# Performance work log

Measured on AMD Instinct MI355X. Metric: run time of the kernel, lower is better.

## Reference

```python
import jax, jax.numpy as jnp
import numpy as np

D = 1024; H = 16; DH = 64; L = 4; N0 = 512; N1 = 512; NF = 16; B = 4; FF = 2730
FUSION = -1; GLOBAL = -2

# static token-type masks (zorro=True path)
_tt = np.concatenate([np.zeros(N0, np.int64), np.ones(N1, np.int64), np.full(NF, FUSION, np.int64)])
_allowed = (_tt[:, None] == _tt[None, :]) | (_tt[:, None] == FUSION)
ATTN_MASK = jnp.asarray(~_allowed)  # True = masked, shape [N, N]
_rt = np.array([0, 1, FUSION, GLOBAL], np.int64)
_pool_allowed = (_rt[:, None] == _tt[None, :]) | (_rt[:, None] == GLOBAL)
POOL_MASK = jnp.asarray(~_pool_allowed)  # [4, N]


def setup_inputs() -> dict:
    key = jax.random.key(0)
    ks = jax.random.split(key, 14)
    s = 0.02
    return {
        'm0': jax.random.normal(ks[0], (B, N0, D), jnp.float32),
        'm1': jax.random.normal(ks[1], (B, N1, D), jnp.float32),
        'fusion_tokens': jax.random.normal(ks[2], (NF, D), jnp.float32),
        'return_tokens': jax.random.normal(ks[3], (4, D), jnp.float32),
        'ln_gamma': jnp.ones((L, D), jnp.float32),
        'wq': jax.random.normal(ks[4], (L, D, H * DH), jnp.float32) * s,
        'wkv': jax.random.normal(ks[5], (L, D, 2 * H * DH), jnp.float32) * s,
        'wo': jax.random.normal(ks[6], (L, H * DH, D), jnp.float32) * s,
        'ff_w1': jax.random.normal(ks[7], (L, D, 2 * FF), jnp.float32) * s,
        'ff_w2': jax.random.normal(ks[8], (L, FF, D), jnp.float32) * s,
        'pool_wq': jax.random.normal(ks[9], (D, H * DH), jnp.float32) * s,
        'pool_wkv': jax.random.normal(ks[10], (D, 2 * H * DH), jnp.float32) * s,
        'pool_wo': jax.random.normal(ks[11], (H * DH, D), jnp.float32) * s,
        'final_gamma': jnp.ones((D,), jnp.float32),
    }


def _ln(x, g):
    mu = jnp.mean(x, axis=-1, keepdims=True)
    var = jnp.mean(jnp.square(x - mu), axis=-1, keepdims=True)
    return (x - mu) * jax.lax.rsqrt(var + 1e-5) * g


def _heads(t):  # [b, n, h*d] -> [b, h, n, d]
    b, n, _ = t.shape
    return t.reshape(b, n, H, DH).transpose(0, 2, 1, 3)


def _attn(x, ctx, wq, wkv, wo, mask):
    q = _heads(x @ wq) * (DH ** -0.5)
    k, v = map(_heads, jnp.split(ctx @ wkv, 2, axis=-1))
    sim = jnp.einsum('bhid,bhjd->bhij', q, k)
    sim = jnp.where(mask, -jnp.finfo(sim.dtype).max, sim)
    attn = jax.nn.softmax(sim, axis=-1)
    out = jnp.einsum('bhij,bhjd->bhid', attn, v)
    b, h, n, d = out.shape
    return out.transpose(0, 2, 1, 3).reshape(b, n, h * d) @ wo


def _ff(x, w1, w2):
    val, gate = jnp.split(x @ w1, 2, axis=-1)
    return (jax.nn.gelu(gate, approximate=False) * val) @ w2


def reference(m0, m1, fusion_tokens, return_tokens, ln_gamma, wq, wkv, wo, ff_w1, ff_w2, pool_wq, pool_wkv, pool_wo, final_gamma):
    b = m0.shape[0]
    fus = jnp.broadcast_to(fusion_tokens[None], (b, NF, D))
    tokens = jnp.concatenate([m0, m1, fus], axis=1)  # [B, N, D]
    for l in range(L):
        h = _ln(tokens, ln_gamma[l])
        tokens = _attn(h, h, wq[l], wkv[l], wo[l], ATTN_MASK) + tokens
        h = _ln(tokens, ln_gamma[l])
        tokens = _ff(h, ff_w1[l], ff_w2[l]) + tokens
    tokens = _ln(tokens, final_gamma)
    q = jnp.broadcast_to(return_tokens[None], (b, 4, D))
    pooled = _attn(q, tokens, pool_wq, pool_wkv, pool_wo, POOL_MASK) + return_tokens[None]
    return pooled
```

## Files before the change

### kernel.cpp

```cpp
#include <hip/hip_runtime.h>
#include <stdint.h>


#define DEV __device__ __forceinline__

typedef unsigned short u16;
typedef __attribute__((ext_vector_type(8))) __bf16 bf16x8;
typedef __attribute__((ext_vector_type(4))) float floatx4;

DEV u16 f2bf(float f) {
  union { float f; unsigned u; } v; v.f = f;
  return (u16)((v.u + 0x7fffu + ((v.u >> 16) & 1u)) >> 16);
}
DEV float bf2f(u16 s) {
  union { unsigned u; float f; } v; v.u = ((unsigned)s) << 16;
  return v.f;
}

#define MFMA(a, b, c) __builtin_amdgcn_mfma_f32_16x16x32_bf16(a, b, c, 0, 0, 0)

DEV void gld16(const u16* g, u16* l) {
  __builtin_amdgcn_global_load_lds((__attribute__((address_space(1))) void*)g,
                                   (__attribute__((address_space(3))) void*)l,
                                   16, 0, 0);
}

DEV int vperm32(int j) {
  return (((j >> 2) & 3) << 3) | (j & 3) | (((j >> 4) & 1) << 2);
}

#define MREAL 4160
#define MPAD  4224
#define NPAD  1056
#define FFP   2816
#define FF2P  5632

__global__ __launch_bounds__(256) void transpose_cvt(
    const float* __restrict__ in, u16* __restrict__ out,
    int Kin, int N, int Kstride) {
  __shared__ float tile[32][33];
  const int k0 = blockIdx.x * 32, n0 = blockIdx.y * 32;
  const int tx = threadIdx.x, ty = threadIdx.y;
#pragma unroll
  for (int i = 0; i < 4; i++) {
    int k = k0 + ty + i * 8;
    tile[ty + i * 8][tx] = (k < Kin) ? in[(int64_t)k * N + n0 + tx] : 0.f;
  }
  __syncthreads();
#pragma unroll
  for (int i = 0; i < 4; i++) {
    int n = n0 + ty + i * 8;
    int k = k0 + tx;
    if (k < Kstride) out[(int64_t)n * Kstride + k] = f2bf(tile[tx][ty + i * 8]);
  }
}

__global__ __launch_bounds__(256) void transpose_w1(
    const float* __restrict__ in, u16* __restrict__ out) {
  __shared__ float tile[32][33];
  const int k0 = blockIdx.x * 32;
  const int r0 = blockIdx.y * 32;
  const int tx = threadIdx.x, ty = threadIdx.y;
  const int vb = (r0 >> 5) << 4;
  const int vi = vb + (tx & 15);
  const int c = (tx < 16) ? vi : 2730 + vi;
  const bool valid = vi < 2730;
#pragma unroll
  for (int i = 0; i < 4; i++) {
    int k = k0 + ty + i * 8;
    tile[ty + i * 8][tx] = valid ? in[(int64_t)k * 5460 + c] : 0.f;
  }
  __syncthreads();
#pragma unroll
  for (int i = 0; i < 4; i++) {
    int rl = ty + i * 8;
    out[(int64_t)(r0 + rl) * 1024 + k0 + tx] = f2bf(tile[tx][rl]);
  }
}

__global__ __launch_bounds__(256) void build_tokens_k(
    const float* __restrict__ m0p, const float* __restrict__ m1p,
    const float* __restrict__ fus, float* __restrict__ tokens) {
  const int n = blockIdx.x, b = blockIdx.y, t = threadIdx.x;
  const float* src = (n < 512) ? m0p + ((int64_t)b * 512 + n) * 1024
                   : (n < 1024) ? m1p + ((int64_t)b * 512 + (n - 512)) * 1024
                                : fus + (int64_t)(n - 1024) * 1024;
  float4 v = ((const float4*)src)[t];
  ((float4*)(tokens + ((int64_t)b * 1040 + n) * 1024))[t] = v;
}

__global__ __launch_bounds__(256) void ln_k(const float* __restrict__ x,
                                            const float* __restrict__ gamma,
                                            u16* __restrict__ out) {
  const int r = blockIdx.x, t = threadIdx.x;
  const float4 v = ((const float4*)(x + (int64_t)r * 1024))[t];
  float s = v.x + v.y + v.z + v.w;
  float q = v.x * v.x + v.y * v.y + v.z * v.z + v.w * v.w;
#pragma unroll
  for (int off = 32; off >= 1; off >>= 1) {
    s += __shfl_xor(s, off);
    q += __shfl_xor(q, off);
  }
  __shared__ float red[8];
  const int w = t >> 6, l = t & 63;
  if (l == 0) { red[w] = s; red[4 + w] = q; }
  __syncthreads();
  s = red[0] + red[1] + red[2] + red[3];
  q = red[4] + red[5] + red[6] + red[7];
  const float mu = s * (1.f / 1024.f);
  const float var = q * (1.f / 1024.f) - mu * mu;
  const float rs = rsqrtf(var + 1e-5f);
  const float4 g = ((const float4*)gamma)[t];
  u16* op = out + (int64_t)r * 1024 + t * 4;
  op[0] = f2bf((v.x - mu) * rs * g.x);
  op[1] = f2bf((v.y - mu) * rs * g.y);
  op[2] = f2bf((v.z - mu) * rs * g.z);
  op[3] = f2bf((v.w - mu) * rs * g.w);
}

enum { EPI_QKV = 0, EPI_KV = 1, EPI_TOKADD = 2, EPI_GG = 3 };

template <int EPI>
__global__ __launch_bounds__(256) void gemm_bt(
    const u16* __restrict__ A, const u16* __restrict__ Bt,
    int Kstr, int Mreal,
    float* __restrict__ tokens, u16* __restrict__ oq, u16* __restrict__ ok,
    u16* __restrict__ ovT, u16* __restrict__ oh2) {
  __shared__ __align__(16) u16 lA[2][128 * 64];
  __shared__ __align__(16) u16 lB[2][128 * 64];
  const int t = threadIdx.x;
  const int w = t >> 6, l = t & 63;
  const int lane16 = l & 15, quad = l >> 4;
  const int m0 = blockIdx.y * 128, n0 = blockIdx.x * 128;
  const int wm = (w >> 1) * 64, wn = (w & 1) * 64;

  const int Klen = Kstr / gridDim.z;
  const int koff = blockIdx.z * Klen;

  const floatx4 fz = {0.f, 0.f, 0.f, 0.f};
  floatx4 acc[4][4];
#pragma unroll
  for (int i = 0; i < 4; i++)
#pragma unroll
    for (int j = 0; j < 4; j++) acc[i][j] = fz;

  const int rowS = t >> 3;
  const int scol = (((t & 7) ^ (rowS & 7)) << 3);
  const u16* gAs = A + (int64_t)(m0 + rowS) * Kstr + koff + scol;
  const u16* gBs = Bt + (int64_t)(n0 + rowS) * Kstr + koff + scol;
  const int64_t csk = (int64_t)32 * Kstr;

  const int rsw = lane16 & 7;
  const int cp0 = ((quad ^ rsw) << 3);
  const int cp1 = (((quad + 4) ^ rsw) << 3);

  auto stage = [&](int buf, int kt) {
    const u16* ga = gAs + kt;
    const u16* gb = gBs + kt;
    u16* la = &lA[buf][0] + t * 8;
    u16* lb = &lB[buf][0] + t * 8;
#pragma unroll
    for (int c = 0; c < 4; c++) {
      gld16(ga + c * csk, la + c * 2048);
      gld16(gb + c * csk, lb + c * 2048);
    }
  };

  stage(0, 0);
  __syncthreads();
  int cur = 0;
  for (int kt = 0; kt < Klen; kt += 64) {
    if (kt + 64 < Klen) stage(cur ^ 1, kt + 64);
    const u16* la = &lA[cur][0] + (wm + lane16) * 64;
    const u16* lb = &lB[cur][0] + (wn + lane16) * 64;
    bf16x8 af[4], bf[4];
#pragma unroll
    for (int i = 0; i < 4; i++) af[i] = *(const bf16x8*)(la + i * 16 * 64 + cp0);
#pragma unroll
    for (int j = 0; j < 4; j++) bf[j] = *(const bf16x8*)(lb + j * 16 * 64 + cp0);
#pragma unroll
    for (int i = 0; i < 4; i++)
#pragma unroll
      for (int j = 0; j < 4; j++) acc[i][j] = MFMA(af[i], bf[j], acc[i][j]);
#pragma unroll
    for (int i = 0; i < 4; i++) af[i] = *(const bf16x8*)(la + i * 16 * 64 + cp1);
#pragma unroll
    for (int j = 0; j < 4; j++) bf[j] = *(const bf16x8*)(lb + j * 16 * 64 + cp1);
#pragma unroll
    for (int i = 0; i < 4; i++)
#pragma unroll
      for (int j = 0; j < 4; j++) acc[i][j] = MFMA(af[i], bf[j], acc[i][j]);
    __syncthreads();
    cur ^= 1;
  }

  if constexpr (EPI == EPI_TOKADD) {
    const bool atomic = gridDim.z > 1;
#pragma unroll
    for (int i = 0; i < 4; i++) {
      const int mb = m0 + wm + i * 16 + quad * 4;
#pragma unroll
      for (int reg = 0; reg < 4; reg++) {
        const int m = mb + reg;
        if (m < Mreal) {
          float* tp = tokens + (int64_t)m * 1024;
#pragma unroll
          for (int j = 0; j < 4; j++) {
            const int n = n0 + wn + j * 16 + lane16;
            if (atomic) atomicAdd(tp + n, acc[i][j][reg]);
            else tp[n] += acc[i][j][reg];
          }
        }
      }
    }
  } else if constexpr (EPI == EPI_QKV) {
#pragma unroll
    for (int i = 0; i < 4; i++) {
      const int mb = m0 + wm + i * 16 + quad * 4;
#pragma unroll
      for (int reg = 0; reg < 4; reg++) {
        const int m = mb + reg;
        if (m < Mreal) {
          const int b = m / 1040, rb = m % 1040;
          const int rbp = (rb & ~31) | vperm32(rb & 31);
#pragma unroll
          for (int j = 0; j < 4; j++) {
            const int n = n0 + wn + j * 16 + lane16;
            const float v = acc[i][j][reg];
            if (n < 1024) {
              const int hd = n >> 6, d = n & 63;
              oq[(((int64_t)b * 16 + hd) * NPAD + rb) * 64 + d] = f2bf(v * 0.125f);
            } else if (n < 2048) {
              const int n2 = n - 1024;
              const int hd = n2 >> 6, d = n2 & 63;
              ok[(((int64_t)b * 16 + hd) * NPAD + rb) * 64 + d] = f2bf(v);
            } else {
              const int n2 = n - 2048;
              const int hd = n2 >> 6, d = n2 & 63;
              ovT[(((int64_t)b * 16 + hd) * 64 + d) * NPAD + rbp] = f2bf(v);
            }
          }
        }
      }
    }
  } else if constexpr (EPI == EPI_KV) {
#pragma unroll
    for (int i = 0; i < 4; i++) {
      const int mb = m0 + wm + i * 16 + quad * 4;
#pragma unroll
      for (int reg = 0; reg < 4; reg++) {
        const int m = mb + reg;
        if (m < Mreal) {
          const int b = m / 1040, rb = m % 1040;
          const int rbp = (rb & ~31) | vperm32(rb & 31);
#pragma unroll
          for (int j = 0; j < 4; j++) {
            const int n = n0 + wn + j * 16 + lane16;
            const float v = acc[i][j][reg];
            if (n < 1024) {
              const int hd = n >> 6, d = n & 63;
              ok[(((int64_t)b * 16 + hd) * NPAD + rb) * 64 + d] = f2bf(v);
            } else {
              const int n2 = n - 1024;
              const int hd = n2 >> 6, d = n2 & 63;
              ovT[(((int64_t)b * 16 + hd) * 64 + d) * NPAD + rbp] = f2bf(v);
            }
          }
        }
      }
    }
  } else {
#pragma unroll
    for (int i = 0; i < 4; i++) {
      const int mb = m0 + wm + i * 16 + quad * 4;
#pragma unroll
      for (int reg = 0; reg < 4; reg++) {
        const int m = mb + reg;
        u16* hp = oh2 + (int64_t)m * FFP;
#pragma unroll
        for (int j = 0; j < 4; j += 2) {
          const float val = acc[i][j][reg];
          const float g = acc[i][j + 1][reg];
          const float ge = 0.5f * g * (1.f + erff(g * 0.70710678118654752f));
          const int vi = (((n0 + wn + j * 16) >> 5) << 4) + lane16;
          hp[vi] = f2bf(val * ge);
        }
      }
    }
  }
}

__global__ __launch_bounds__(256) void attn_k(const u16* __restrict__ qb,
                                              const u16* __restrict__ kb,
                                              const u16* __restrict__ vTb,
                                              u16* __restrict__ ao) {
  const int t = threadIdx.x, w = t >> 6, l = t & 63;
  const int lane16 = l & 15, quad = l >> 4;
  const int kvb = quad * 4;
  const int bh = blockIdx.y, b = bh >> 4, h = bh & 15;
  const int row0 = blockIdx.x * 64 + w * 16;
  if (row0 >= 1040) return;
  const int type = (row0 < 512) ? 0 : (row0 < 1024 ? 1 : 2);
  const int cbeg = (type == 1) ? 512 : 0;
  const int cend = (type == 0) ? 512 : (type == 1 ? 1024 : 1040);
  const int niter = (cend - cbeg + 31) >> 5;

  const u16* qp = qb + ((int64_t)bh * NPAD + row0 + lane16) * 64 + quad * 8;
  const bf16x8 a0 = *(const bf16x8*)qp;
  const bf16x8 a1 = *(const bf16x8*)(qp + 32);
  const u16* vbase = vTb + ((int64_t)bh * 64 + lane16) * NPAD + quad * 8;

  const floatx4 fz = {0.f, 0.f, 0.f, 0.f};
  floatx4 O[4] = {fz, fz, fz, fz};
  float mrow = -1e30f, lrow = 0.f;

  for (int it = 0; it < niter; ++it) {
    const int c0 = cbeg + it * 32;
    const u16* kp = kb + ((int64_t)bh * NPAD + c0 + lane16) * 64 + quad * 8;
    const bf16x8 b00 = *(const bf16x8*)kp;
    const bf16x8 b01 = *(const bf16x8*)(kp + 32);
    const bf16x8 b10 = *(const bf16x8*)(kp + 16 * 64);
    const bf16x8 b11 = *(const bf16x8*)(kp + 16 * 64 + 32);
    floatx4 s0 = MFMA(b00, a0, fz); s0 = MFMA(b01, a1, s0);
    floatx4 s1 = MFMA(b10, a0, fz); s1 = MFMA(b11, a1, s1);
    if (c0 + 32 > cend) {
#pragma unroll
      for (int r = 0; r < 4; r++) {
        if (c0 + kvb + r >= cend) s0[r] = -1e30f;
        if (c0 + 16 + kvb + r >= cend) s1[r] = -1e30f;
      }
    }
    float tm = fmaxf(fmaxf(fmaxf(s0[0], s0[1]), fmaxf(s0[2], s0[3])),
                     fmaxf(fmaxf(s1[0], s1[1]), fmaxf(s1[2], s1[3])));
    tm = fmaxf(tm, __shfl_xor(tm, 16));
    tm = fmaxf(tm, __shfl_xor(tm, 32));
    if (!__all(tm <= mrow)) {
      const float mn = fmaxf(mrow, tm);
      const float a_ = __expf(mrow - mn);
      mrow = mn;
      lrow *= a_;
      const float al0 = __shfl(a_, kvb + 0, 16);
      const float al1 = __shfl(a_, kvb + 1, 16);
      const float al2 = __shfl(a_, kvb + 2, 16);
      const float al3 = __shfl(a_, kvb + 3, 16);
#pragma unroll
      for (int dt = 0; dt < 4; dt++) {
        O[dt][0] *= al0; O[dt][1] *= al1; O[dt][2] *= al2; O[dt][3] *= al3;
      }
    }
    float p0[4], p1[4];
#pragma unroll
    for (int r = 0; r < 4; r++) {
      p0[r] = __expf(s0[r] - mrow);
      p1[r] = __expf(s1[r] - mrow);
    }
    float ps = ((p0[0] + p0[1]) + (p0[2] + p0[3])) +
               ((p1[0] + p1[1]) + (p1[2] + p1[3]));
    ps += __shfl_xor(ps, 16);
    ps += __shfl_xor(ps, 32);
    lrow += ps;
    union { bf16x8 v; u16 s[8]; } pf;
#pragma unroll
    for (int r = 0; r < 4; r++) {
      pf.s[r] = f2bf(p0[r]);
      pf.s[4 + r] = f2bf(p1[r]);
    }
#pragma unroll
    for (int dt = 0; dt < 4; dt++) {
      const bf16x8 bv = *(const bf16x8*)(vbase + (int64_t)dt * 16 * NPAD + c0);
      O[dt] = MFMA(pf.v, bv, O[dt]);
    }
  }
  float lr[4];
#pragma unroll
  for (int r = 0; r < 4; r++) lr[r] = __shfl(lrow, kvb + r, 16);
#pragma unroll
  for (int dt = 0; dt < 4; dt++)
#pragma unroll
    for (int r = 0; r < 4; r++) {
      const int row = row0 + kvb + r;
      ao[((int64_t)b * 1040 + row) * 1024 + h * 64 + dt * 16 + lane16] =
          f2bf(O[dt][r] / lr[r]);
    }
}

__global__ __launch_bounds__(256) void poolq_k(const float* __restrict__ rtk,
                                               const float* __restrict__ pwq,
                                               u16* __restrict__ qP) {
  const int r = blockIdx.y;
  const int n = blockIdx.x * 256 + threadIdx.x;
  if (r >= 4) { qP[(int64_t)r * 1024 + n] = 0; return; }
  const float* x = rtk + (int64_t)r * 1024;
  float acc = 0.f;
#pragma unroll 8
  for (int k = 0; k < 1024; k++) acc += x[k] * pwq[(int64_t)k * 1024 + n];
  qP[(int64_t)r * 1024 + n] = f2bf(acc * 0.125f);
}

DEV bool pvalid(int r, int c) {
  if (r == 0) return c < 512;
  if (r == 1) return (c >= 512) && (c < 1024);
  if (r == 2) return (c >= 1024) && (c < 1040);
  return c < 1040;
}

__global__ __launch_bounds__(64) void pool_attn_k(const u16* __restrict__ qP,
                                                  const u16* __restrict__ kb,
                                                  const u16* __restrict__ vTb,
                                                  u16* __restrict__ po) {
  const int l = threadIdx.x;
  const int lane16 = l & 15, quad = l >> 4;
  const int kvb = quad * 4;
  const int bh = blockIdx.x, b = bh >> 4, h = bh & 15;
  const u16* qp = qP + (int64_t)lane16 * 1024 + h * 64 + quad * 8;
  const bf16x8 a0 = *(const bf16x8*)qp;
  const bf16x8 a1 = *(const bf16x8*)(qp + 32);
  const u16* vbase = vTb + ((int64_t)bh * 64 + lane16) * NPAD + quad * 8;
  const floatx4 fz = {0.f, 0.f, 0.f, 0.f};
  floatx4 O[4] = {fz, fz, fz, fz};
  float mrow = -1e30f, lrow = 0.f;
  for (int it = 0; it < 33; ++it) {
    const int c0 = it * 32;
    const u16* kp = kb + ((int64_t)bh * NPAD + c0 + lane16) * 64 + quad * 8;
    const bf16x8 b00 = *(const bf16x8*)kp;
    const bf16x8 b01 = *(const bf16x8*)(kp + 32);
    const bf16x8 b10 = *(const bf16x8*)(kp + 16 * 64);
    const bf16x8 b11 = *(const bf16x8*)(kp + 16 * 64 + 32);
    floatx4 s0 = MFMA(b00, a0, fz); s0 = MFMA(b01, a1, s0);
    floatx4 s1 = MFMA(b10, a0, fz); s1 = MFMA(b11, a1, s1);
#pragma unroll
    for (int r = 0; r < 4; r++) {
      if (!pvalid(lane16, c0 + kvb + r)) s0[r] = -1e30f;
      if (!pvalid(lane16, c0 + 16 + kvb + r)) s1[r] = -1e30f;
    }
    float tm = fmaxf(fmaxf(fmaxf(s0[0], s0[1]), fmaxf(s0[2], s0[3])),
                     fmaxf(fmaxf(s1[0], s1[1]), fmaxf(s1[2], s1[3])));
    tm = fmaxf(tm, __shfl_xor(tm, 16));
    tm = fmaxf(tm, __shfl_xor(tm, 32));
    if (!__all(tm <= mrow)) {
      const float mn = fmaxf(mrow, tm);
      const float a_ = __expf(mrow - mn);
      mrow = mn;
      lrow *= a_;
      const float al0 = __shfl(a_, kvb + 0, 16);
      const float al1 = __shfl(a_, kvb + 1, 16);
      const float al2 = __shfl(a_, kvb + 2, 16);
      const float al3 = __shfl(a_, kvb + 3, 16);
#pragma unroll
      for (int dt = 0; dt < 4; dt++) {
        O[dt][0] *= al0; O[dt][1] *= al1; O[dt][2] *= al2; O[dt][3] *= al3;
      }
    }
    float p0[4], p1[4];
#pragma unroll
    for (int r = 0; r < 4; r++) {
      p0[r] = __expf(s0[r] - mrow);
      p1[r] = __expf(s1[r] - mrow);
    }
    float ps = ((p0[0] + p0[1]) + (p0[2] + p0[3])) +
               ((p1[0] + p1[1]) + (p1[2] + p1[3]));
    ps += __shfl_xor(ps, 16);
    ps += __shfl_xor(ps, 32);
    lrow += ps;
    union { bf16x8 v; u16 s[8]; } pf;
#pragma unroll
    for (int r = 0; r < 4; r++) {
      pf.s[r] = f2bf(p0[r]);
      pf.s[4 + r] = f2bf(p1[r]);
    }
#pragma unroll
    for (int dt = 0; dt < 4; dt++) {
      const bf16x8 bv = *(const bf16x8*)(vbase + (int64_t)dt * 16 * NPAD + c0);
      O[dt] = MFMA(pf.v, bv, O[dt]);
    }
  }
  float lr[4];
#pragma unroll
  for (int r = 0; r < 4; r++) lr[r] = __shfl(lrow, r, 16);
  if (quad == 0) {
#pragma unroll
    for (int dt = 0; dt < 4; dt++)
#pragma unroll
      for (int r = 0; r < 4; r++)
        po[((int64_t)b * 4 + r) * 1024 + h * 64 + dt * 16 + lane16] =
            f2bf(O[dt][r] / lr[r]);
  }
}

__global__ __launch_bounds__(256) void fout_k(const u16* __restrict__ po,
                                              const float* __restrict__ pwo,
                                              const float* __restrict__ rtk,
                                              float* __restrict__ out) {
  const int row = blockIdx.y;
  const int n = blockIdx.x * 256 + threadIdx.x;
  const u16* x = po + (int64_t)row * 1024;
  float acc = 0.f;
#pragma unroll 8
  for (int k = 0; k < 1024; k++) acc += bf2f(x[k]) * pwo[(int64_t)k * 1024 + n];
  out[(int64_t)row * 1024 + n] = acc + rtk[(int64_t)(row & 3) * 1024 + n];
}

extern "C" void kernel_launch(void* const* d_in, const int* in_sizes, int n_in,
                              void* d_out, int out_size, void* d_ws, size_t ws_size,
                              hipStream_t stream) {
  (void)in_sizes; (void)n_in; (void)out_size; (void)ws_size;
  const float* m0p  = (const float*)d_in[0];
  const float* m1p  = (const float*)d_in[1];
  const float* fus  = (const float*)d_in[2];
  const float* rtk  = (const float*)d_in[3];
  const float* lng  = (const float*)d_in[4];
  const float* wq   = (const float*)d_in[5];
  const float* wkv  = (const float*)d_in[6];
  const float* wo   = (const float*)d_in[7];
  const float* w1   = (const float*)d_in[8];
  const float* w2   = (const float*)d_in[9];
  const float* pwq  = (const float*)d_in[10];
  const float* pwkv = (const float*)d_in[11];
  const float* pwo  = (const float*)d_in[12];
  const float* fg   = (const float*)d_in[13];
  float* out = (float*)d_out;

  char* p = (char*)d_ws;
  auto alloc = [&](size_t bytes) -> char* {
    char* r = p;
    p += (bytes + 255) & ~(size_t)255;
    return r;
  };
  u16* warena = (u16*)alloc((size_t)FF2P * 1024 * 2);
  float* tokens = (float*)alloc((size_t)MREAL * 1024 * 4);
  u16* hbuf  = (u16*)alloc((size_t)MPAD * 1024 * 2);
  u16* qb    = (u16*)alloc((size_t)64 * NPAD * 64 * 2);
  u16* kbuf  = (u16*)alloc((size_t)64 * NPAD * 64 * 2);
  u16* vTbuf = (u16*)alloc((size_t)64 * NPAD * 64 * 2);
  u16* h2buf = qb;
  u16* qP    = (u16*)alloc((size_t)16 * 1024 * 2);
  u16* poolO = (u16*)alloc((size_t)16 * 1024 * 2);

  const dim3 tb(32, 8, 1);
  build_tokens_k<<<dim3(1040, 4), 256, 0, stream>>>(m0p, m1p, fus, tokens);

  for (int lyr = 0; lyr < 4; ++lyr) {
    ln_k<<<MREAL, 256, 0, stream>>>(tokens, lng + lyr * 1024, hbuf);
    transpose_cvt<<<dim3(32, 32), tb, 0, stream>>>(
        wq + (int64_t)lyr * 1024 * 1024, warena, 1024, 1024, 1024);
    transpose_cvt<<<dim3(32, 64), tb, 0, stream>>>(
        wkv + (int64_t)lyr * 1024 * 2048, warena + (size_t)1024 * 1024, 1024, 2048, 1024);
    gemm_bt<EPI_QKV><<<dim3(24, 33), 256, 0, stream>>>(
        hbuf, warena, 1024, MREAL, nullptr, qb, kbuf, vTbuf, nullptr);
    attn_k<<<dim3(17, 64), 256, 0, stream>>>(qb, kbuf, vTbuf, hbuf);
    transpose_cvt<<<dim3(32, 32), tb, 0, stream>>>(
        wo + (int64_t)lyr * 1024 * 1024, warena, 1024, 1024, 1024);
    gemm_bt<EPI_TOKADD><<<dim3(8, 33, 2), 256, 0, stream>>>(
        hbuf, warena, 1024, MREAL, tokens, nullptr, nullptr, nullptr, nullptr);
    ln_k<<<MREAL, 256, 0, stream>>>(tokens, lng + lyr * 1024, hbuf);
    transpose_w1<<<dim3(32, FF2P / 32), tb, 0, stream>>>(
        w1 + (int64_t)lyr * 1024 * 5460, warena);
    gemm_bt<EPI_GG><<<dim3(FF2P / 128, 33), 256, 0, stream>>>(
        hbuf, warena, 1024, MREAL, nullptr, nullptr, nullptr, nullptr, h2buf);
    transpose_cvt<<<dim3(FFP / 32, 32), tb, 0, stream>>>(
        w2 + (int64_t)lyr * 2730 * 1024, warena, 2730, 1024, FFP);
    gemm_bt<EPI_TOKADD><<<dim3(8, 33, 2), 256, 0, stream>>>(
        h2buf, warena, FFP, MREAL, tokens, nullptr, nullptr, nullptr, nullptr);
  }

  ln_k<<<MREAL, 256, 0, stream>>>(tokens, fg, hbuf);
  transpose_cvt<<<dim3(32, 64), tb, 0, stream>>>(pwkv, warena, 1024, 2048, 1024);
  gemm_bt<EPI_KV><<<dim3(16, 33), 256, 0, stream>>>(
      hbuf, warena, 1024, MREAL, nullptr, nullptr, kbuf, vTbuf, nullptr);
  poolq_k<<<dim3(4, 16), 256, 0, stream>>>(rtk, pwq, qP);
  pool_attn_k<<<64, 64, 0, stream>>>(qP, kbuf, vTbuf, poolO);
  fout_k<<<dim3(4, 16), 256, 0, stream>>>(poolO, pwo, rtk, out);
}
```

Baseline: 1.877 ms.

## Replace atomic split-K residual adds with delta buffers fused into LayerNorm

The split-K output and FF-down GEMMs now write plain partial results into separate delta buffers instead of atomically adding into the residual tokens. A new add_ln_k kernel sums the tokens with the deltas, writes the updated residual back, and applies the next LayerNorm in one pass. This is meant to remove atomic read-modify-write traffic and a separate residual read. In exchange it needs extra workspace and adds extra fp32 reads and writes, and it falls back to the old path when the workspace is too small.

Measured after the change: 1.802 ms. -4.0%, faster.

```diff
diff --git a/kernel.cpp b/kernel.cpp
--- a/kernel.cpp
+++ b/kernel.cpp
@@ -118,7 +118,47 @@
   op[3] = f2bf((v.w - mu) * rs * g.w);
 }
 
-enum { EPI_QKV = 0, EPI_KV = 1, EPI_TOKADD = 2, EPI_GG = 3 };
+__global__ __launch_bounds__(256) void add_ln_k(
+    float* __restrict__ x, const float* __restrict__ d0,
+    const float* __restrict__ d1, const float* __restrict__ gamma,
+    u16* __restrict__ out, int two, int writeback) {
+  const int r = blockIdx.x, t = threadIdx.x;
+  const int64_t off = (int64_t)r * 1024 + t * 4;
+  float4 v = *(const float4*)(x + off);
+  {
+    const float4 a = *(const float4*)(d0 + off);
+    v.x += a.x; v.y += a.y; v.z += a.z; v.w += a.w;
+  }
+  if (two) {
+    const float4 a = *(const float4*)(d1 + off);
+    v.x += a.x; v.y += a.y; v.z += a.z; v.w += a.w;
+  }
+  if (writeback) *(float4*)(x + off) = v;
+  float s = v.x + v.y + v.z + v.w;
+  float q = v.x * v.x + v.y * v.y + v.z * v.z + v.w * v.w;
+#pragma unroll
+  for (int off2 = 32; off2 >= 1; off2 >>= 1) {
+    s += __shfl_xor(s, off2);
+    q += __shfl_xor(q, off2);
+  }
+  __shared__ float red[8];
+  const int w = t >> 6, l = t & 63;
+  if (l == 0) { red[w] = s; red[4 + w] = q; }
+  __syncthreads();
+  s = red[0] + red[1] + red[2] + red[3];
+  q = red[4] + red[5] + red[6] + red[7];
+  const float mu = s * (1.f / 1024.f);
+  const float var = q * (1.f / 1024.f) - mu * mu;
+  const float rs = rsqrtf(var + 1e-5f);
+  const float4 g = ((const float4*)gamma)[t];
+  u16* op = out + (int64_t)r * 1024 + t * 4;
+  op[0] = f2bf((v.x - mu) * rs * g.x);
+  op[1] = f2bf((v.y - mu) * rs * g.y);
+  op[2] = f2bf((v.z - mu) * rs * g.z);
+  op[3] = f2bf((v.w - mu) * rs * g.w);
+}
+
+enum { EPI_QKV = 0, EPI_KV = 1, EPI_TOKADD = 2, EPI_GG = 3, EPI_DELTA = 4 };
 
 template <int EPI>
 __global__ __launch_bounds__(256) void gemm_bt(
@@ -209,6 +249,24 @@
             const int n = n0 + wn + j * 16 + lane16;
             if (atomic) atomicAdd(tp + n, acc[i][j][reg]);
             else tp[n] += acc[i][j][reg];
+          }
+        }
+      }
+    }
+  } else if constexpr (EPI == EPI_DELTA) {
+    float* dp = tokens + (int64_t)blockIdx.z * MREAL * 1024;
+#pragma unroll
+    for (int i = 0; i < 4; i++) {
+      const int mb = m0 + wm + i * 16 + quad * 4;
+#pragma unroll
+      for (int reg = 0; reg < 4; reg++) {
+        const int m = mb + reg;
+        if (m < Mreal) {
+          float* tp = dp + (int64_t)m * 1024;
+#pragma unroll
+          for (int j = 0; j < 4; j++) {
+            const int n = n0 + wn + j * 16 + lane16;
+            tp[n] = acc[i][j][reg];
           }
         }
       }
@@ -503,7 +561,7 @@
 extern "C" void kernel_launch(void* const* d_in, const int* in_sizes, int n_in,
                               void* d_out, int out_size, void* d_ws, size_t ws_size,
                               hipStream_t stream) {
-  (void)in_sizes; (void)n_in; (void)out_size; (void)ws_size;
+  (void)in_sizes; (void)n_in; (void)out_size;
   const float* m0p  = (const float*)d_in[0];
   const float* m1p  = (const float*)d_in[1];
   const float* fus  = (const float*)d_in[2];
@@ -536,34 +594,83 @@
   u16* qP    = (u16*)alloc((size_t)16 * 1024 * 2);
   u16* poolO = (u16*)alloc((size_t)16 * 1024 * 2);
 
+  const size_t DELTA_BYTES = (size_t)MREAL * 1024 * 4;
+  const size_t base_used = (size_t)(p - (char*)d_ws);
+  int mode = 0;
+  float* d0 = nullptr;
+  float* d1 = nullptr;
+  if (ws_size >= base_used + 2 * DELTA_BYTES + 1024) {
+    mode = 2;
+    d0 = (float*)alloc(2 * DELTA_BYTES);
+    d1 = d0 + (size_t)MREAL * 1024;
+  } else if (ws_size >= base_used + DELTA_BYTES + 1024) {
+    mode = 1;
+    d0 = (float*)alloc(DELTA_BYTES);
+    d1 = d0;
+  }
+
   const dim3 tb(32, 8, 1);
   build_tokens_k<<<dim3(1040, 4), 256, 0, stream>>>(m0p, m1p, fus, tokens);
 
-  for (int lyr = 0; lyr < 4; ++lyr) {
-    ln_k<<<MREAL, 256, 0, stream>>>(tokens, lng + lyr * 1024, hbuf);
-    transpose_cvt<<<dim3(32, 32), tb, 0, stream>>>(
-        wq + (int64_t)lyr * 1024 * 1024, warena, 1024, 1024, 1024);
-    transpose_cvt<<<dim3(32, 64), tb, 0, stream>>>(
-        wkv + (int64_t)lyr * 1024 * 2048, warena + (size_t)1024 * 1024, 1024, 2048, 1024);
-    gemm_bt<EPI_QKV><<<dim3(24, 33), 256, 0, stream>>>(
-        hbuf, warena, 1024, MREAL, nullptr, qb, kbuf, vTbuf, nullptr);
-    attn_k<<<dim3(17, 64), 256, 0, stream>>>(qb, kbuf, vTbuf, hbuf);
-    transpose_cvt<<<dim3(32, 32), tb, 0, stream>>>(
-        wo + (int64_t)lyr * 1024 * 1024, warena, 1024, 1024, 1024);
-    gemm_bt<EPI_TOKADD><<<dim3(8, 33, 2), 256, 0, stream>>>(
-        hbuf, warena, 1024, MREAL, tokens, nullptr, nullptr, nullptr, nullptr);
-    ln_k<<<MREAL, 256, 0, stream>>>(tokens, lng + lyr * 1024, hbuf);
-    transpose_w1<<<dim3(32, FF2P / 32), tb, 0, stream>>>(
-        w1 + (int64_t)lyr * 1024 * 5460, warena);
-    gemm_bt<EPI_GG><<<dim3(FF2P / 128, 33), 256, 0, stream>>>(
-        hbuf, warena, 1024, MREAL, nullptr, nullptr, nullptr, nullptr, h2buf);
-    transpose_cvt<<<dim3(FFP / 32, 32), tb, 0, stream>>>(
-        w2 + (int64_t)lyr * 2730 * 1024, warena, 2730, 1024, FFP);
-    gemm_bt<EPI_TOKADD><<<dim3(8, 33, 2), 256, 0, stream>>>(
-        h2buf, warena, FFP, MREAL, tokens, nullptr, nullptr, nullptr, nullptr);
-  }
-
-  ln_k<<<MREAL, 256, 0, stream>>>(tokens, fg, hbuf);
+  if (mode) {
+    const int zz = mode;
+    const int two = (mode == 2);
+    for (int lyr = 0; lyr < 4; ++lyr) {
+      if (lyr == 0)
+        ln_k<<<MREAL, 256, 0, stream>>>(tokens, lng, hbuf);
+      else
+        add_ln_k<<<MREAL, 256, 0, stream>>>(tokens, d0, d1, lng + lyr * 1024,
+                                            hbuf, two, 1);
+      transpose_cvt<<<dim3(32, 32), tb, 0, stream>>>(
+          wq + (int64_t)lyr * 1024 * 1024, warena, 1024, 1024, 1024);
+      transpose_cvt<<<dim3(32, 64), tb, 0, stream>>>(
+          wkv + (int64_t)lyr * 1024 * 2048, warena + (size_t)1024 * 1024, 1024, 2048, 1024);
+      gemm_bt<EPI_QKV><<<dim3(24, 33), 256, 0, stream>>>(
+          hbuf, warena, 1024, MREAL, nullptr, qb, kbuf, vTbuf, nullptr);
+      attn_k<<<dim3(17, 64), 256, 0, stream>>>(qb, kbuf, vTbuf, hbuf);
+      transpose_cvt<<<dim3(32, 32), tb, 0, stream>>>(
+          wo + (int64_t)lyr * 1024 * 1024, warena, 1024, 1024, 1024);
+      gemm_bt<EPI_DELTA><<<dim3(8, 33, zz), 256, 0, stream>>>(
+          hbuf, warena, 1024, MREAL, d0, nullptr, nullptr, nullptr, nullptr);
+      add_ln_k<<<MREAL, 256, 0, stream>>>(tokens, d0, d1, lng + lyr * 1024,
+                                          hbuf, two, 1);
+      transpose_w1<<<dim3(32, FF2P / 32), tb, 0, stream>>>(
+          w1 + (int64_t)lyr * 1024 * 5460, warena);
+      gemm_bt<EPI_GG><<<dim3(FF2P / 128, 33), 256, 0, stream>>>(
+          hbuf, warena, 1024, MREAL, nullptr, nullptr, nullptr, nullptr, h2buf);
+      transpose_cvt<<<dim3(FFP / 32, 32), tb, 0, stream>>>(
+          w2 + (int64_t)lyr * 2730 * 1024, warena, 2730, 1024, FFP);
+      gemm_bt<EPI_DELTA><<<dim3(8, 33, zz), 256, 0, stream>>>(
+          h2buf, warena, FFP, MREAL, d0, nullptr, nullptr, nullptr, nullptr);
+    }
+    add_ln_k<<<MREAL, 256, 0, stream>>>(tokens, d0, d1, fg, hbuf, two, 0);
+  } else {
+    for (int lyr = 0; lyr < 4; ++lyr) {
+      ln_k<<<MREAL, 256, 0, stream>>>(tokens, lng + lyr * 1024, hbuf);
+      transpose_cvt<<<dim3(32, 32), tb, 0, stream>>>(
+          wq + (int64_t)lyr * 1024 * 1024, warena, 1024, 1024, 1024);
+      transpose_cvt<<<dim3(32, 64), tb, 0, stream>>>(
+          wkv + (int64_t)lyr * 1024 * 2048, warena + (size_t)1024 * 1024, 1024, 2048, 1024);
+      gemm_bt<EPI_QKV><<<dim3(24, 33), 256, 0, stream>>>(
+          hbuf, warena, 1024, MREAL, nullptr, qb, kbuf, vTbuf, nullptr);
+      attn_k<<<dim3(17, 64), 256, 0, stream>>>(qb, kbuf, vTbuf, hbuf);
+      transpose_cvt<<<dim3(32, 32), tb, 0, stream>>>(
+          wo + (int64_t)lyr * 1024 * 1024, warena, 1024, 1024, 1024);
+      gemm_bt<EPI_TOKADD><<<dim3(8, 33, 2), 256, 0, stream>>>(
+          hbuf, warena, 1024, MREAL, tokens, nullptr, nullptr, nullptr, nullptr);
+      ln_k<<<MREAL, 256, 0, stream>>>(tokens, lng + lyr * 1024, hbuf);
+      transpose_w1<<<dim3(32, FF2P / 32), tb, 0, stream>>>(
+          w1 + (int64_t)lyr * 1024 * 5460, warena);
+      gemm_bt<EPI_GG><<<dim3(FF2P / 128, 33), 256, 0, stream>>>(
+          hbuf, warena, 1024, MREAL, nullptr, nullptr, nullptr, nullptr, h2buf);
+      transpose_cvt<<<dim3(FFP / 32, 32), tb, 0, stream>>>(
+          w2 + (int64_t)lyr * 2730 * 1024, warena, 2730, 1024, FFP);
+      gemm_bt<EPI_TOKADD><<<dim3(8, 33, 2), 256, 0, stream>>>(
+          h2buf, warena, FFP, MREAL, tokens, nullptr, nullptr, nullptr, nullptr);
+    }
+    ln_k<<<MREAL, 256, 0, stream>>>(tokens, fg, hbuf);
+  }
+
   transpose_cvt<<<dim3(32, 64), tb, 0, stream>>>(pwkv, warena, 1024, 2048, 1024);
   gemm_bt<EPI_KV><<<dim3(16, 33), 256, 0, stream>>>(
       hbuf, warena, 1024, MREAL, nullptr, nullptr, kbuf, vTbuf, nullptr);
```
